# Performance work log

Measured on AMD Instinct MI355X. Metric: run time of the kernel, lower is better.

## Reference

```python
import jax, jax.numpy as jnp
import numpy as np

EPS = 1e-6
LAMB = 0.05
NEG = -1000.0


def setup_inputs() -> dict:
    key = jax.random.key(0)
    k1, k2, k3, k4, k5, k6 = jax.random.split(key, 6)
    Bi, Bt, K, L, D = 128, 128, 36, 64, 1024
    imgs = jax.random.normal(k1, (Bi, K, D), dtype=jnp.float32)
    caps = jax.random.normal(k2, (Bt, L, D), dtype=jnp.float32)
    img_cls = jax.random.normal(k3, (Bi, D), dtype=jnp.float32)
    cap_cls = jax.random.normal(k4, (Bt, D), dtype=jnp.float32)
    # variable lengths; pin one element to max so torch's [:, :max] slice is identity
    img_lens = jax.random.randint(k5, (Bi,), K // 2, K + 1).astype(jnp.int32).at[0].set(K)
    cap_lens = jax.random.randint(k6, (Bt,), L // 2, L + 1).astype(jnp.int32).at[0].set(L)
    return {"img_cls": img_cls, "imgs": imgs, "cap_cls": cap_cls,
            "caps": caps, "img_lens": img_lens, "cap_lens": cap_lens}


def reference(img_cls, imgs, cap_cls, caps, img_lens, cap_lens):
    # HiCHAN.forward_cam (img_cls / cap_cls unused by this branch)
    imgs = imgs + EPS
    caps = caps + EPS
    imgs = imgs / jnp.linalg.norm(imgs, axis=-1, keepdims=True)
    caps = caps / jnp.linalg.norm(caps, axis=-1, keepdims=True)

    K, L = imgs.shape[1], caps.shape[1]
    # fine-grained similarity tensor [Bi, Bt, K, L]
    fg_sims = jnp.einsum('ikd,tld->itkl', imgs, caps)

    # fg mask: valid region k of image i AND valid word l of caption t
    img_valid = jnp.arange(K)[None, :] < img_lens[:, None]      # [Bi, K]
    cap_valid = jnp.arange(L)[None, :] < cap_lens[:, None]      # [Bt, L]
    mask = img_valid[:, None, :, None] & cap_valid[None, :, None, :]  # [Bi,Bt,K,L] bool
    m = mask.astype(fg_sims.dtype)

    # masked temperature softmax (single scores tensor reused for both axes)
    scores = jnp.where(mask, fg_sims, NEG) / LAMB
    v2t_attn = jax.nn.softmax(scores, axis=-1)
    v2t = jnp.sum(v2t_attn * fg_sims * m, axis=-1)   # [Bi,Bt,K]
    t2v_attn = jax.nn.softmax(scores, axis=-2)
    t2v = jnp.sum(t2v_attn * fg_sims * m, axis=-2)   # [Bi,Bt,L]

    # _ave_init: uniform weights over valid rows / cols
    r_b = mask.any(axis=-1).astype(fg_sims.dtype)    # [Bi,Bt,K]
    c_b = mask.any(axis=-2).astype(fg_sims.dtype)    # [Bi,Bt,L]
    r = r_b / r_b.sum(axis=-1, keepdims=True)
    c = c_b / c_b.sum(axis=-1, keepdims=True)

    sims = (jnp.sum(v2t * r, axis=-1) + jnp.sum(t2v * c, axis=-1)) / 2  # [Bi,Bt]
    return sims
```

## Files before the change

kernel.cpp:

```cpp
#include <hip/hip_runtime.h>
#include <stdint.h>

#define BI 128
#define BT 128
#define KIMG 36
#define LCAP 64
#define DD 1024
#define MP 48
#define MB 96
#define NB 256
#define ASLOTS 384
#define ABYTES 6144
#define STG_BYTES 22528

typedef _Float16 h4 __attribute__((ext_vector_type(4)));
typedef _Float16 h8 __attribute__((ext_vector_type(8)));
typedef float f4 __attribute__((ext_vector_type(4)));

__device__ __forceinline__ float wave_red_sum(float v) {
#pragma unroll
  for (int o = 1; o < 64; o <<= 1) v += __shfl_xor(v, o, 64);
  return v;
}
__device__ __forceinline__ float wave_red_max(float v) {
#pragma unroll
  for (int o = 1; o < 64; o <<= 1) v = fmaxf(v, __shfl_xor(v, o, 64));
  return v;
}

__global__ __launch_bounds__(256) void norm_kernel(
    const float* __restrict__ imgs, const float* __restrict__ caps,
    _Float16* __restrict__ Ah, _Float16* __restrict__ Bh) {
  int row = blockIdx.x;
  int tid = threadIdx.x;
  const float* src;
  _Float16* dst;
  if (row < BI * MP) {
    int i = row / MP, k = row - i * MP;
    dst = Ah + (size_t)row * DD;
    if (k >= KIMG) {
      h4 z = {};
      ((h4*)dst)[tid] = z;
      return;
    }
    src = imgs + ((size_t)i * KIMG + k) * DD;
  } else {
    int r = row - BI * MP;
    dst = Bh + (size_t)r * DD;
    src = caps + (size_t)r * DD;
  }
  float4 x = ((const float4*)src)[tid];
  x.x += 1e-6f; x.y += 1e-6f; x.z += 1e-6f; x.w += 1e-6f;
  float ss = x.x * x.x + x.y * x.y + x.z * x.z + x.w * x.w;
  ss = wave_red_sum(ss);
  __shared__ float red[4];
  int lane = tid & 63, w = tid >> 6;
  if (lane == 0) red[w] = ss;
  __syncthreads();
  float scale = rsqrtf(red[0] + red[1] + red[2] + red[3]);
  h4 o;
  o[0] = (_Float16)(x.x * scale);
  o[1] = (_Float16)(x.y * scale);
  o[2] = (_Float16)(x.z * scale);
  o[3] = (_Float16)(x.w * scale);
  ((h4*)dst)[tid] = o;
}

__global__ __launch_bounds__(256, 3) void sims_kernel(
    const _Float16* __restrict__ Ah, const _Float16* __restrict__ Bh,
    const int* __restrict__ img_lens, const int* __restrict__ cap_lens,
    float* __restrict__ out) {
  __shared__ char stage[2 * STG_BYTES] __attribute__((aligned(16)));

  int tid = threadIdx.x;
  int lane = tid & 63;
  int w = tid >> 6;

  int wgid = blockIdx.x;
  int xcd = wgid & 7;
  int slot = wgid >> 3;
  int bx = 4 * xcd + (slot & 3);
  int by = slot >> 2;

  int fr = lane & 15;
  int fq = lane >> 4;

  const size_t arow0 = (size_t)by * MB;
  const size_t brow0 = (size_t)bx * NB;

  int c0 = 6 * w - ((w >> 1) & (w & 1));
  int nch = (w < 2) ? 6 : 5;
  int s0 = c0 * 64 + lane;
  bool isA = (w == 0);
  int srel = isA ? s0 : s0 - ASLOTS;
  int sw0 = srel ^ ((srel >> 3) & 7);
  const _Float16* gp0 =
      (isA ? Ah + arow0 * DD : Bh + brow0 * DD) + (size_t)(sw0 >> 2) * DD + (sw0 & 3) * 8;
  const int lds0 = c0 * 1024 + lane * 16;

  int aoff[6], boff[4];
#pragma unroll
  for (int mi = 0; mi < 6; ++mi) {
    int s = (16 * mi + fr) * 4 + fq;
    aoff[mi] = (s ^ ((s >> 3) & 7)) * 16;
  }
#pragma unroll
  for (int ni = 0; ni < 4; ++ni) {
    int s = (64 * w + 16 * ni + fr) * 4 + fq;
    boff[ni] = ABYTES + (s ^ ((s >> 3) & 7)) * 16;
  }

  auto STAGE = [&](int buf, int k0) {
#pragma unroll
    for (int it = 0; it < 6; ++it) {
      if (it < nch) {
        __builtin_amdgcn_global_load_lds(
            (const __attribute__((address_space(1))) void*)(gp0 + (size_t)it * 16 * DD + k0),
            (__attribute__((address_space(3))) void*)(stage + buf * STG_BYTES + lds0 + it * 1024),
            16, 0, 0);
      }
    }
  };

  f4 acc[6][4] = {};

  STAGE(0, 0);
  __syncthreads();

  for (int t = 0; t < 32; ++t) {
    const char* rb = stage + (t & 1) * STG_BYTES;
    if (t < 31) STAGE((t + 1) & 1, 32 * (t + 1));
    h8 af[6], bf[4];
#pragma unroll
    for (int mi = 0; mi < 6; ++mi)
      af[mi] = *(const h8*)(rb + aoff[mi]);
#pragma unroll
    for (int ni = 0; ni < 4; ++ni)
      bf[ni] = *(const h8*)(rb + boff[ni]);
#pragma unroll
    for (int mi = 0; mi < 6; ++mi)
#pragma unroll
      for (int ni = 0; ni < 4; ++ni)
        acc[mi][ni] = __builtin_amdgcn_mfma_f32_16x16x32_f16(
            af[mi], bf[ni], acc[mi][ni], 0, 0, 0);
    __syncthreads();
  }

  int t = bx * 4 + w;
  int Lt = cap_lens[t];

#pragma unroll
  for (int img = 0; img < 2; ++img) {
    int Ki = img_lens[2 * by + img];

    float m = -1e30f;
#pragma unroll
    for (int mi = 0; mi < 3; ++mi)
#pragma unroll
      for (int ni = 0; ni < 4; ++ni)
#pragma unroll
        for (int j = 0; j < 4; ++j) {
          bool valid = (16 * mi + 4 * fq + j < Ki) && (16 * ni + fr < Lt);
          if (valid) m = fmaxf(m, acc[3 * img + mi][ni][j]);
        }
    m = wave_red_max(m);

    float rowe[3][4] = {}, rowes[3][4] = {}, cole[4] = {}, coles[4] = {};
#pragma unroll
    for (int mi = 0; mi < 3; ++mi)
#pragma unroll
      for (int ni = 0; ni < 4; ++ni)
#pragma unroll
        for (int j = 0; j < 4; ++j) {
          float s = acc[3 * img + mi][ni][j];
          bool valid = (16 * mi + 4 * fq + j < Ki) && (16 * ni + fr < Lt);
          float e = valid ? __expf((s - m) * 20.0f) : 0.f;
          float es = e * s;
          rowe[mi][j] += e;
          rowes[mi][j] += es;
          cole[ni] += e;
          coles[ni] += es;
        }

    float part = 0.f;
#pragma unroll
    for (int mi = 0; mi < 3; ++mi)
#pragma unroll
      for (int j = 0; j < 4; ++j) {
        float Re = rowe[mi][j], Res = rowes[mi][j];
#pragma unroll
        for (int o = 1; o < 16; o <<= 1) {
          Re += __shfl_xor(Re, o, 64);
          Res += __shfl_xor(Res, o, 64);
        }
        int row = 16 * mi + 4 * fq + j;
        if (fr == 0 && row < Ki) part += (Res / Re) * (0.5f / (float)Ki);
      }
#pragma unroll
    for (int ni = 0; ni < 4; ++ni) {
      float Ce = cole[ni], Ces = coles[ni];
#pragma unroll
      for (int o = 16; o < 64; o <<= 1) {
        Ce += __shfl_xor(Ce, o, 64);
        Ces += __shfl_xor(Ces, o, 64);
      }
      int l = 16 * ni + fr;
      if (fq == 0 && l < Lt) part += (Ces / Ce) * (0.5f / (float)Lt);
    }
    float sim = wave_red_sum(part);
    if (lane == 0) out[(size_t)(2 * by + img) * BT + t] = sim;
  }
}

extern "C" void kernel_launch(void* const* d_in, const int* in_sizes, int n_in,
                              void* d_out, int out_size, void* d_ws, size_t ws_size,
                              hipStream_t stream) {
  const float* imgs = (const float*)d_in[1];
  const float* caps = (const float*)d_in[3];
  const int* img_lens = (const int*)d_in[4];
  const int* cap_lens = (const int*)d_in[5];
  float* out = (float*)d_out;

  _Float16* Ah = (_Float16*)d_ws;
  _Float16* Bh = Ah + (size_t)BI * MP * DD;

  norm_kernel<<<BI * MP + BT * LCAP, 256, 0, stream>>>(imgs, caps, Ah, Bh);
  sims_kernel<<<2048, 256, 0, stream>>>(Ah, Bh, img_lens, cap_lens, out);
}
```

Measured before the change: 150.8 us.

## Load B fragments directly from a pre-tiled global layout into registers

The norm kernel now writes caption rows in an MFMA-fragment-tiled layout, so each wave can load its B operands straight from global memory into registers with one contiguous 16-byte load per lane. Only the A tile is still staged through LDS, which cuts LDS use per block from about 44KB to 12KB and removes LDS traffic for B. B fragments are double-buffered in registers and the MFMA block is wrapped in s_setprio. In exchange, every wave fetches its own B data from global or L2 memory rather than sharing it through LDS, and the extra register buffers may reduce occupancy.

```diff
diff --git a/kernel.cpp b/kernel.cpp
--- a/kernel.cpp
+++ b/kernel.cpp
@@ -9,9 +9,7 @@
 #define MP 48
 #define MB 96
 #define NB 256
-#define ASLOTS 384
-#define ABYTES 6144
-#define STG_BYTES 22528
+#define ABUF 6144
 
 typedef _Float16 h4 __attribute__((ext_vector_type(4)));
 typedef _Float16 h8 __attribute__((ext_vector_type(8)));
@@ -34,19 +32,20 @@
   int row = blockIdx.x;
   int tid = threadIdx.x;
   const float* src;
-  _Float16* dst;
+  bool isCap;
+  int r = 0;
   if (row < BI * MP) {
     int i = row / MP, k = row - i * MP;
-    dst = Ah + (size_t)row * DD;
+    isCap = false;
     if (k >= KIMG) {
       h4 z = {};
-      ((h4*)dst)[tid] = z;
+      ((h4*)(Ah + (size_t)row * DD))[tid] = z;
       return;
     }
     src = imgs + ((size_t)i * KIMG + k) * DD;
   } else {
-    int r = row - BI * MP;
-    dst = Bh + (size_t)r * DD;
+    r = row - BI * MP;
+    isCap = true;
     src = caps + (size_t)r * DD;
   }
   float4 x = ((const float4*)src)[tid];
@@ -63,14 +62,21 @@
   o[1] = (_Float16)(x.y * scale);
   o[2] = (_Float16)(x.z * scale);
   o[3] = (_Float16)(x.w * scale);
-  ((h4*)dst)[tid] = o;
+  if (!isCap) {
+    ((h4*)(Ah + (size_t)row * DD))[tid] = o;
+  } else {
+    int k = 4 * tid;
+    size_t tile = (size_t)(r >> 4) * 32 + (k >> 5);
+    int sub = ((k >> 3) & 3) * 128 + (r & 15) * 8 + (k & 7);
+    *(h4*)(Bh + tile * 512 + sub) = o;
+  }
 }
 
 __global__ __launch_bounds__(256, 3) void sims_kernel(
     const _Float16* __restrict__ Ah, const _Float16* __restrict__ Bh,
     const int* __restrict__ img_lens, const int* __restrict__ cap_lens,
     float* __restrict__ out) {
-  __shared__ char stage[2 * STG_BYTES] __attribute__((aligned(16)));
+  __shared__ char stage[2 * ABUF] __attribute__((aligned(16)));
 
   int tid = threadIdx.x;
   int lane = tid & 63;
@@ -88,62 +94,65 @@
   const size_t arow0 = (size_t)by * MB;
   const size_t brow0 = (size_t)bx * NB;
 
-  int c0 = 6 * w - ((w >> 1) & (w & 1));
-  int nch = (w < 2) ? 6 : 5;
+  const int c0 = (w < 2) ? 2 * w : w + 2;
+  const int nch = (w < 2) ? 2 : 1;
   int s0 = c0 * 64 + lane;
-  bool isA = (w == 0);
-  int srel = isA ? s0 : s0 - ASLOTS;
-  int sw0 = srel ^ ((srel >> 3) & 7);
-  const _Float16* gp0 =
-      (isA ? Ah + arow0 * DD : Bh + brow0 * DD) + (size_t)(sw0 >> 2) * DD + (sw0 & 3) * 8;
+  int sw0 = s0 ^ ((s0 >> 3) & 7);
+  const _Float16* gpA = Ah + (arow0 + (sw0 >> 2)) * DD + (sw0 & 3) * 8;
   const int lds0 = c0 * 1024 + lane * 16;
 
-  int aoff[6], boff[4];
-#pragma unroll
-  for (int mi = 0; mi < 6; ++mi) {
-    int s = (16 * mi + fr) * 4 + fq;
-    aoff[mi] = (s ^ ((s >> 3) & 7)) * 16;
-  }
-#pragma unroll
-  for (int ni = 0; ni < 4; ++ni) {
-    int s = (64 * w + 16 * ni + fr) * 4 + fq;
-    boff[ni] = ABYTES + (s ^ ((s >> 3) & 7)) * 16;
-  }
+  int sl = 4 * fr + fq;
+  const int aoff0 = (sl ^ ((sl >> 3) & 7)) * 16;
+
+  const _Float16* bp[4];
+#pragma unroll
+  for (int ni = 0; ni < 4; ++ni)
+    bp[ni] = Bh + ((size_t)((bx * 16) + 4 * w + ni) * 32) * 512 + lane * 8;
+
+  f4 acc[6][4] = {};
+  h8 bfA[4], bfB[4];
 
   auto STAGE = [&](int buf, int k0) {
-#pragma unroll
-    for (int it = 0; it < 6; ++it) {
-      if (it < nch) {
-        __builtin_amdgcn_global_load_lds(
-            (const __attribute__((address_space(1))) void*)(gp0 + (size_t)it * 16 * DD + k0),
-            (__attribute__((address_space(3))) void*)(stage + buf * STG_BYTES + lds0 + it * 1024),
-            16, 0, 0);
-      }
+    __builtin_amdgcn_global_load_lds(
+        (const __attribute__((address_space(1))) void*)(gpA + k0),
+        (__attribute__((address_space(3))) void*)(stage + buf * ABUF + lds0), 16, 0, 0);
+    if (nch == 2)
+      __builtin_amdgcn_global_load_lds(
+          (const __attribute__((address_space(1))) void*)(gpA + 16 * DD + k0),
+          (__attribute__((address_space(3))) void*)(stage + buf * ABUF + lds0 + 1024), 16, 0, 0);
+  };
+  auto LOADB = [&](h8(&bf)[4], int t) {
+#pragma unroll
+    for (int ni = 0; ni < 4; ++ni) bf[ni] = *(const h8*)(bp[ni] + 512 * t);
+  };
+  auto BODY = [&](int t, int parity, h8(&cur)[4], h8(&nxt)[4]) {
+    if (t < 31) {
+      STAGE(parity ^ 1, 32 * (t + 1));
+      LOADB(nxt, t + 1);
     }
-  };
-
-  f4 acc[6][4] = {};
-
-  STAGE(0, 0);
-  __syncthreads();
-
-  for (int t = 0; t < 32; ++t) {
-    const char* rb = stage + (t & 1) * STG_BYTES;
-    if (t < 31) STAGE((t + 1) & 1, 32 * (t + 1));
-    h8 af[6], bf[4];
+    const char* rb = stage + parity * ABUF;
+    h8 af[6];
 #pragma unroll
     for (int mi = 0; mi < 6; ++mi)
-      af[mi] = *(const h8*)(rb + aoff[mi]);
-#pragma unroll
-    for (int ni = 0; ni < 4; ++ni)
-      bf[ni] = *(const h8*)(rb + boff[ni]);
+      af[mi] = *(const h8*)(rb + aoff0 + 1024 * mi);
+    __builtin_amdgcn_s_setprio(1);
 #pragma unroll
     for (int mi = 0; mi < 6; ++mi)
 #pragma unroll
       for (int ni = 0; ni < 4; ++ni)
         acc[mi][ni] = __builtin_amdgcn_mfma_f32_16x16x32_f16(
-            af[mi], bf[ni], acc[mi][ni], 0, 0, 0);
+            af[mi], cur[ni], acc[mi][ni], 0, 0, 0);
+    __builtin_amdgcn_s_setprio(0);
     __syncthreads();
+  };
+
+  STAGE(0, 0);
+  LOADB(bfA, 0);
+  __syncthreads();
+
+  for (int tt = 0; tt < 32; tt += 2) {
+    BODY(tt, 0, bfA, bfB);
+    BODY(tt + 1, 1, bfB, bfA);
   }
 
   int t = bx * 4 + w;
```

New measurement: 141.2 us. 1.07x faster.
